# Kernel optimization log

Measured on AMD Instinct MI355X. Metric: run time of the kernel, lower is better.

The kernel has to match this reference:

```python
import jax, jax.numpy as jnp
import numpy as np
from jax import lax

NGTH = 15  # num_gth_mem
EPS = 1e-5  # BatchNorm eps


def _conv(x, w, b):
    y = lax.conv_general_dilated(x, w, (1, 1), 'VALID',
                                 dimension_numbers=('NCHW', 'OIHW', 'NCHW'))
    return y + b[None, :, None, None]


def _bn(x, g, b, m, v):
    # eval-mode BatchNorm2d with running stats
    return g[None, :, None, None] * (x - m[None, :, None, None]) * lax.rsqrt(v[None, :, None, None] + EPS) + b[None, :, None, None]


def _masked_stats(x, w):
    # x: (B, M, ...) ; w: (B, M) float weights. Population mean/std over masked mem slots.
    extra = (1,) * (x.ndim - 2)
    we = w.reshape(w.shape[:2] + extra)
    cnt = jnp.sum(w, axis=1).reshape((w.shape[0],) + extra)
    s = jnp.sum(x * we, axis=1)
    ss = jnp.sum(x * x * we, axis=1)
    mean = s / cnt
    var = jnp.maximum(ss / cnt - mean * mean, 0.0)
    return mean, jnp.sqrt(var)


def _forward(target_scores, ptm, pmt, predicted_iou, mem_mask, params):
    nf, ns, nmem, c, h, w = ptm.shape
    B = nf * ns
    ts = target_scores.reshape(B, 1, h, w)
    pmt = pmt.reshape(B, nmem, 1, h, w)
    ptm = ptm.reshape(B, nmem, c, h, w)
    mask = mem_mask.reshape(B, nmem)
    piou = predicted_iou.reshape(B, 1, 1, 1)

    mf = mask.astype(ts.dtype)
    # rank of each selected slot within the masked (ordered) selection
    rank = jnp.cumsum(mf, axis=1) - 1.0
    gth_w = mf * (rank < NGTH).astype(ts.dtype)   # first NGTH selected slots
    oth_w = mf * (rank >= NGTH).astype(ts.dtype)  # remaining selected slots

    max_ts = jnp.max(ts.reshape(B, -1), axis=1)

    pmt_mean, pmt_std = _masked_stats(pmt, mf)                 # (B,1,h,w)
    pmt_gth = pmt[:, :NGTH]                                    # unmasked slice (as in torch code)
    pmt_gth_mean = jnp.mean(pmt_gth, axis=1)
    pmt_gth_std = jnp.std(pmt_gth, axis=1)
    pmt_oth_mean, pmt_oth_std = _masked_stats(pmt, oth_w)

    ptm_max = jnp.max(ptm.reshape(B, nmem, -1), axis=2)        # (B, nmem)
    m_mm, s_mm = _masked_stats(ptm_max, mf)
    m_gm, s_gm = _masked_stats(ptm_max, gth_w)
    m_om, s_om = _masked_stats(ptm_max, oth_w)

    def bcast(v):
        return jnp.broadcast_to(v.reshape(B, 1, 1, 1), (B, 1, h, w))

    inp = jnp.concatenate([
        bcast(max_ts), jnp.broadcast_to(piou, (B, 1, h, w)),
        pmt_mean, pmt_std, pmt_gth_mean, pmt_gth_std, pmt_oth_mean, pmt_oth_std,
        bcast(m_mm), bcast(s_mm), bcast(m_gm), bcast(s_gm), bcast(m_om), bcast(s_om)
    ], axis=1)  # (B, 14, h, w)

    (c1w, c1b, g1, b1, m1, v1, c2w, c2b, g2, b2, m2, v2,
     c3w, c3b, g3, b3, m3, v3, c4w, c4b) = params
    x = jax.nn.relu(_bn(_conv(inp, c1w, c1b), g1, b1, m1, v1))
    x = lax.reduce_window(x, -jnp.inf, lax.max, (1, 1, 2, 2), (1, 1, 2, 2), 'VALID')
    x = jax.nn.relu(_bn(_conv(x, c2w, c2b), g2, b2, m2, v2))
    x = jax.nn.relu(_bn(_conv(x, c3w, c3b), g3, b3, m3, v3))
    x = _conv(x, c4w, c4b)
    return jnp.max(x, axis=(2, 3), keepdims=True)  # AdaptiveMaxPool2d((1,1)) -> (B,1,1,1)


def setup_inputs() -> dict:
    key = jax.random.key(0)
    ks = jax.random.split(key, 16)
    nf, ns, nmem, h, w = 16, 32, 30, 32, 32
    d = {}
    d['target_scores'] = jax.random.normal(ks[0], (nf, ns, 1, h, w), jnp.float32)
    d['ptm'] = jax.random.uniform(ks[1], (nf, ns, nmem, 1, h, w), jnp.float32)
    d['pmt'] = jax.random.uniform(ks[2], (nf, ns, nmem, 1, h, w), jnp.float32)
    d['predicted_iou'] = jax.random.uniform(ks[3], (nf, ns), jnp.float32)
    mask = jax.random.uniform(ks[4], (nf, ns, nmem)) < 0.7
    mask = mask.at[..., :20].set(True)  # >= 20 selected -> 'other' set non-empty
    d['mem_mask'] = mask
    d['conv1_w'] = jax.random.normal(ks[5], (64, 14, 3, 3), jnp.float32) * 0.1
    d['conv1_b'] = jnp.zeros((64,), jnp.float32)
    d['bn1_g'] = jnp.ones((64,), jnp.float32); d['bn1_b'] = jnp.zeros((64,), jnp.float32)
    d['bn1_m'] = jnp.zeros((64,), jnp.float32); d['bn1_v'] = jnp.ones((64,), jnp.float32)
    d['conv2_w'] = jax.random.normal(ks[6], (64, 64, 3, 3), jnp.float32) * 0.05
    d['conv2_b'] = jnp.zeros((64,), jnp.float32)
    d['bn2_g'] = jnp.ones((64,), jnp.float32); d['bn2_b'] = jnp.zeros((64,), jnp.float32)
    d['bn2_m'] = jnp.zeros((64,), jnp.float32); d['bn2_v'] = jnp.ones((64,), jnp.float32)
    d['conv3_w'] = jax.random.normal(ks[7], (64, 64, 3, 3), jnp.float32) * 0.05
    d['conv3_b'] = jnp.zeros((64,), jnp.float32)
    d['bn3_g'] = jnp.ones((64,), jnp.float32); d['bn3_b'] = jnp.zeros((64,), jnp.float32)
    d['bn3_m'] = jnp.zeros((64,), jnp.float32); d['bn3_v'] = jnp.ones((64,), jnp.float32)
    d['conv4_w'] = jax.random.normal(ks[8], (1, 64, 3, 3), jnp.float32) * 0.05
    d['conv4_b'] = jnp.zeros((1,), jnp.float32)
    return d


def reference(target_scores, ptm, pmt, predicted_iou, mem_mask,
              conv1_w, conv1_b, bn1_g, bn1_b, bn1_m, bn1_v,
              conv2_w, conv2_b, bn2_g, bn2_b, bn2_m, bn2_v,
              conv3_w, conv3_b, bn3_g, bn3_b, bn3_m, bn3_v,
              conv4_w, conv4_b):
    params = (conv1_w, conv1_b, bn1_g, bn1_b, bn1_m, bn1_v,
              conv2_w, conv2_b, bn2_g, bn2_b, bn2_m, bn2_v,
              conv3_w, conv3_b, bn3_g, bn3_b, bn3_m, bn3_v,
              conv4_w, conv4_b)
    return _forward(target_scores, ptm, pmt, predicted_iou, mem_mask, params)
```

## Files before the change

kernel.cpp:

```cpp
#include <hip/hip_runtime.h>
#include <math.h>

#define NFB  512
#define NMEM 30
#define PIX  1024
#define EPSF 1e-5f

typedef _Float16 half8_t __attribute__((ext_vector_type(8)));
typedef _Float16 half4_t __attribute__((ext_vector_type(4)));
typedef float float4_t __attribute__((ext_vector_type(4)));

#define OFF_SCAL  8388608
#define OFF_PMAX  8413184
#define OFF_WPAIR 8474624
#define OFF_X1H   8597504
#define OFF_X2H   24326144
#define OFF_X3H   37957632
#define OFF_W2R   49491968
#define OFF_W3R   49565696
#define OFF_WR1   49639424
#define OFF_WSUM1 49651712

__global__ __launch_bounds__(256) void k_repack(
    const float* __restrict__ w, _Float16* __restrict__ wr)
{
  int i = blockIdx.x * 256 + threadIdx.x;
  if (i < 36864) {
    int kr = i / 12288;
    int rem = i - kr * 12288;
    int oc = rem / 192;
    int k = rem - oc * 192;
    int kc = k >> 6, ci = k & 63;
    wr[i] = (_Float16)w[((oc * 64 + ci) * 3 + kr) * 3 + kc];
  }
}

__global__ __launch_bounds__(256) void k_repack1(
    const float* __restrict__ w, _Float16* __restrict__ wr1,
    float* __restrict__ wsum1)
{
  int i = blockIdx.x * 256 + threadIdx.x;
  if (i < 6144) {
    int kr = i / 2048;
    int rem = i - kr * 2048;
    int oc = rem >> 5;
    int k = rem & 31;
    int kc = k >> 3, ci = k & 7;
    _Float16 v = (_Float16)0.f;
    if (kc < 3 && ci < 6)
      v = (_Float16)w[((oc * 14 + (2 + ci)) * 3 + kr) * 3 + kc];
    wr1[i] = v;
  } else if (i < 6144 + 512) {
    int j = i - 6144;
    int oc = j >> 3, u = j & 7;
    const int uch[8] = {0, 1, 8, 9, 10, 11, 12, 13};
    const float* wp = w + (oc * 14 + uch[u]) * 9;
    float s = 0.f;
    #pragma unroll
    for (int k = 0; k < 9; ++k) s += wp[k];
    wsum1[j] = s;
  }
}

__global__ __launch_bounds__(256) void kA_ptm_max(
    const float* __restrict__ ptm, float* __restrict__ pmax)
{
  const int t = threadIdx.x, lane = t & 63, wave = t >> 6;
  const int w = blockIdx.x * 4 + wave;
  const float* p = ptm + (size_t)w * PIX;
  float4 v0 = *(const float4*)(p + lane * 4);
  float4 v1 = *(const float4*)(p + lane * 4 + 256);
  float4 v2 = *(const float4*)(p + lane * 4 + 512);
  float4 v3 = *(const float4*)(p + lane * 4 + 768);
  float mx = fmaxf(fmaxf(fmaxf(v0.x, v0.y), fmaxf(v0.z, v0.w)),
                   fmaxf(fmaxf(v1.x, v1.y), fmaxf(v1.z, v1.w)));
  mx = fmaxf(mx, fmaxf(fmaxf(fmaxf(v2.x, v2.y), fmaxf(v2.z, v2.w)),
                       fmaxf(fmaxf(v3.x, v3.y), fmaxf(v3.z, v3.w))));
  #pragma unroll
  for (int off = 32; off > 0; off >>= 1)
    mx = fmaxf(mx, __shfl_down(mx, off, 64));
  if (lane == 0) pmax[w] = mx;
}

__global__ __launch_bounds__(256) void kB_scal(
    const float* __restrict__ ts, const float* __restrict__ piou,
    const int* __restrict__ mask, const float* __restrict__ pmax,
    float* __restrict__ scal12, float2* __restrict__ wpair)
{
  const int b = blockIdx.x, t = threadIdx.x, lane = t & 63, wave = t >> 6;
  __shared__ float s_red[4];
  {
    float4 v = ((const float4*)(ts + (size_t)b * PIX))[t];
    float mx = fmaxf(fmaxf(v.x, v.y), fmaxf(v.z, v.w));
    #pragma unroll
    for (int off = 32; off > 0; off >>= 1)
      mx = fmaxf(mx, __shfl_down(mx, off, 64));
    if (lane == 0) s_red[wave] = mx;
  }
  __syncthreads();
  if (t == 0) {
    float maxts = fmaxf(fmaxf(s_red[0], s_red[1]), fmaxf(s_red[2], s_red[3]));
    float wm[NMEM], wo[NMEM];
    float cum = 0.f, cm = 0.f, cg = 0.f, co = 0.f;
    #pragma unroll
    for (int m = 0; m < NMEM; ++m) {
      float f  = (mask[b * NMEM + m] != 0) ? 1.f : 0.f;
      float gg = (cum < 15.f) ? f : 0.f;
      float oo = f - gg;
      cum += f;
      wm[m] = f; wo[m] = oo;
      cm += f; cg += gg; co += oo;
    }
    const float* px = pmax + b * NMEM;
    float sm = 0, sm2 = 0, sg = 0, sg2 = 0, so = 0, so2 = 0;
    #pragma unroll
    for (int m = 0; m < NMEM; ++m) {
      float x = px[m];
      float gg = wm[m] - wo[m];
      sm += wm[m] * x;  sm2 += wm[m] * x * x;
      sg += gg * x;     sg2 += gg * x * x;
      so += wo[m] * x;  so2 += wo[m] * x * x;
      wpair[b * NMEM + m] = make_float2(wm[m], wo[m]);
    }
    float a = sm / cm, g = sg / cg, o = so / co;
    float* sp = scal12 + b * 12;
    sp[0] = maxts; sp[1] = piou[b];
    sp[2] = a; sp[3] = sqrtf(fmaxf(sm2 / cm - a * a, 0.f));
    sp[4] = g; sp[5] = sqrtf(fmaxf(sg2 / cg - g * g, 0.f));
    sp[6] = o; sp[7] = sqrtf(fmaxf(so2 / co - o * o, 0.f));
    sp[8] = cm; sp[9] = cg; sp[10] = co; sp[11] = 0.f;
  }
}

__global__ __launch_bounds__(256) void kC_pmt_stats(
    const float* __restrict__ pmt, const float2* __restrict__ wpair,
    const float* __restrict__ scal12, _Float16* __restrict__ img6h)
{
  const int b = blockIdx.x, t = threadIdx.x;
  __shared__ float s_wm[NMEM], s_wo[NMEM];
  if (t < NMEM) {
    float2 wv = wpair[b * NMEM + t];
    s_wm[t] = wv.x; s_wo[t] = wv.y;
  }
  __syncthreads();
  const float cm = scal12[b * 12 + 8];
  const float co = scal12[b * 12 + 10];
  const int p0 = t * 4;
  const float* pb = pmt + (size_t)b * NMEM * PIX + p0;

  float sA[4] = {0,0,0,0}, qA[4] = {0,0,0,0};
  float sG[4] = {0,0,0,0}, qG[4] = {0,0,0,0};
  float sO[4] = {0,0,0,0}, qO[4] = {0,0,0,0};

  #pragma unroll 1
  for (int mb = 0; mb < 15; mb += 5) {
    float4 v[5];
    #pragma unroll
    for (int j = 0; j < 5; ++j) v[j] = *(const float4*)(pb + (size_t)(mb + j) * PIX);
    #pragma unroll
    for (int j = 0; j < 5; ++j) {
      float wm = s_wm[mb + j], wo = s_wo[mb + j];
      float xv[4] = {v[j].x, v[j].y, v[j].z, v[j].w};
      #pragma unroll
      for (int k = 0; k < 4; ++k) {
        float x = xv[k];
        sA[k] = fmaf(wm, x, sA[k]); qA[k] = fmaf(wm * x, x, qA[k]);
        sO[k] = fmaf(wo, x, sO[k]); qO[k] = fmaf(wo * x, x, qO[k]);
        sG[k] += x; qG[k] = fmaf(x, x, qG[k]);
      }
    }
  }
  #pragma unroll 1
  for (int mb = 15; mb < 30; mb += 5) {
    float4 v[5];
    #pragma unroll
    for (int j = 0; j < 5; ++j) v[j] = *(const float4*)(pb + (size_t)(mb + j) * PIX);
    #pragma unroll
    for (int j = 0; j < 5; ++j) {
      float wm = s_wm[mb + j], wo = s_wo[mb + j];
      float xv[4] = {v[j].x, v[j].y, v[j].z, v[j].w};
      #pragma unroll
      for (int k = 0; k < 4; ++k) {
        float x = xv[k];
        sA[k] = fmaf(wm, x, sA[k]); qA[k] = fmaf(wm * x, x, qA[k]);
        sO[k] = fmaf(wo, x, sO[k]); qO[k] = fmaf(wo * x, x, qO[k]);
      }
    }
  }

  half8_t* ob = (half8_t*)(img6h + (size_t)b * 8192 + (size_t)p0 * 8);
  #pragma unroll
  for (int j = 0; j < 4; ++j) {
    float m0 = sA[j] / cm;   float d0 = sqrtf(fmaxf(qA[j] / cm - m0 * m0, 0.f));
    float m1 = sG[j] / 15.f; float d1 = sqrtf(fmaxf(qG[j] / 15.f - m1 * m1, 0.f));
    float m2 = sO[j] / co;   float d2 = sqrtf(fmaxf(qO[j] / co - m2 * m2, 0.f));
    half8_t v;
    v[0] = (_Float16)m0; v[1] = (_Float16)d0;
    v[2] = (_Float16)m1; v[3] = (_Float16)d1;
    v[4] = (_Float16)m2; v[5] = (_Float16)d2;
    v[6] = (_Float16)0.f; v[7] = (_Float16)0.f;
    ob[j] = v;
  }
}

__global__ __launch_bounds__(256) void k1_conv1_mfma(
    const _Float16* __restrict__ img6h, const float* __restrict__ scal12,
    const _Float16* __restrict__ wr1, const float* __restrict__ wsum1,
    const float* __restrict__ bias, const float* __restrict__ gam,
    const float* __restrict__ bet, const float* __restrict__ mu,
    const float* __restrict__ var, _Float16* __restrict__ x1h)
{
  __shared__ _Float16 s_img[1028 * 8];
  const int b = blockIdx.x, t = threadIdx.x, lane = t & 63, wave = t >> 6;
  const int n16 = lane & 15, q = lane >> 4;
  {
    const half8_t* src = (const half8_t*)(img6h + (size_t)b * 8192);
    half8_t* dst = (half8_t*)s_img;
    for (int i = t; i < 1024; i += 256) dst[i] = src[i];
    if (t < 4) {
      half8_t z = {(_Float16)0.f, (_Float16)0.f, (_Float16)0.f, (_Float16)0.f,
                   (_Float16)0.f, (_Float16)0.f, (_Float16)0.f, (_Float16)0.f};
      dst[1024 + t] = z;
    }
  }

  const int ocA = wave * 16 + n16;
  half8_t af[3];
  #pragma unroll
  for (int kr = 0; kr < 3; ++kr)
    af[kr] = *(const half8_t*)(wr1 + (kr * 64 + ocA) * 32 + q * 8);

  const int oc0 = wave * 16 + q * 4;
  float scv[4], shv[4], cst[4];
  {
    const float* sp = scal12 + b * 12;
    #pragma unroll
    for (int rg = 0; rg < 4; ++rg) {
      int oc = oc0 + rg;
      float s = gam[oc] * rsqrtf(var[oc] + EPSF);
      scv[rg] = s;
      shv[rg] = (bias[oc] - mu[oc]) * s + bet[oc];
      float c = 0.f;
      #pragma unroll
      for (int u = 0; u < 8; ++u) c = fmaf(wsum1[oc * 8 + u], sp[u], c);
      cst[rg] = c;
    }
  }
  __syncthreads();

  #pragma unroll 1
  for (int pr = 0; pr < 15; ++pr) {
    const int r0 = pr * 2;
    float4_t acc[2][2];
    #pragma unroll
    for (int row = 0; row < 2; ++row)
      #pragma unroll
      for (int tt = 0; tt < 2; ++tt)
        acc[row][tt] = (float4_t){0.f, 0.f, 0.f, 0.f};
    #pragma unroll
    for (int row = 0; row < 2; ++row) {
      #pragma unroll
      for (int kr = 0; kr < 3; ++kr) {
        const int ip = (r0 + row + kr) * 32 + n16 + q;
        #pragma unroll
        for (int tt = 0; tt < 2; ++tt) {
          half8_t bf = *(const half8_t*)(s_img + (ip + tt * 16) * 8);
          acc[row][tt] = __builtin_amdgcn_mfma_f32_16x16x32_f16(
              af[kr], bf, acc[row][tt], 0, 0, 0);
        }
      }
    }
    #pragma unroll
    for (int tt = 0; tt < 2; ++tt) {
      float mm[4];
      #pragma unroll
      for (int j = 0; j < 4; ++j) {
        float m = fmaxf(acc[0][tt][j], acc[1][tt][j]);
        mm[j] = fmaxf(m, __shfl_xor(m, 1, 64));
      }
      if ((n16 & 1) == 0) {
        int pc = tt * 8 + (n16 >> 1);
        half4_t v;
        if (pc < 15) {
          #pragma unroll
          for (int rg = 0; rg < 4; ++rg)
            v[rg] = (_Float16)fmaxf(scv[rg] * (mm[rg] + cst[rg]) + shv[rg], 0.f);
        } else {
          v[0] = (_Float16)0.f; v[1] = (_Float16)0.f;
          v[2] = (_Float16)0.f; v[3] = (_Float16)0.f;
        }
        *(half4_t*)(x1h + ((((size_t)b * 15 + pr) * 16) + pc) * 64 + oc0) = v;
      }
    }
  }
}

template<int IH, int OW, int NT>
__global__ __launch_bounds__(256, 3) void k_conv_mfma(
    const _Float16* __restrict__ xin, const _Float16* __restrict__ wrep,
    const float* __restrict__ bias, const float* __restrict__ gam,
    const float* __restrict__ bet, const float* __restrict__ mu,
    const float* __restrict__ var, _Float16* __restrict__ xout)
{
  constexpr int NPIX = OW * OW;
  constexpr int NIN = IH * 16;
  __shared__ _Float16 s_in[NIN * 72 + 8];
  const int b = blockIdx.x, t = threadIdx.x;
  const int lane = t & 63, wave = t >> 6;
  const int n16 = lane & 15, q = lane >> 4;

  {
    const half8_t* src = (const half8_t*)(xin + (size_t)b * NIN * 64);
    half8_t* dst = (half8_t*)s_in;
    for (int g = t; g < NIN * 8; g += 256) {
      int pix = g >> 3, cib = g & 7;
      dst[pix * 9 + cib] = src[g];
    }
  }

  int base72[NT];
  #pragma unroll
  for (int nt = 0; nt < NT; ++nt) {
    int p = nt * 16 + n16;
    int pe = (p < NPIX) ? p : (NPIX - 1);
    int r = pe / OW, c = pe - r * OW;
    base72[nt] = (r * 16 + c) * 72;
  }

  float4_t acc[NT];
  #pragma unroll
  for (int nt = 0; nt < NT; ++nt) acc[nt] = (float4_t){0.f, 0.f, 0.f, 0.f};

  const int ocA = wave * 16 + n16;
  __syncthreads();

  #pragma unroll 1
  for (int kr = 0; kr < 3; ++kr) {
    half8_t af[6];
    const half8_t* wp = (const half8_t*)(wrep + (size_t)(kr * 64 + ocA) * 192 + q * 8);
    #pragma unroll
    for (int ks = 0; ks < 6; ++ks) af[ks] = wp[ks * 4];
    const int krbase = kr * (16 * 72);
    #pragma unroll
    for (int ks = 0; ks < 6; ++ks) {
      const int k0 = ks * 32 + q * 8;
      const int kadd = krbase + (k0 >> 6) * 72 + (k0 & 63);
      #pragma unroll
      for (int nt = 0; nt < NT; ++nt) {
        half8_t bf = *(const half8_t*)(s_in + base72[nt] + kadd);
        acc[nt] = __builtin_amdgcn_mfma_f32_16x16x32_f16(af[ks], bf, acc[nt], 0, 0, 0);
      }
    }
  }

  const int ocb = wave * 16 + q * 4;
  float scv[4], shv[4];
  #pragma unroll
  for (int rg = 0; rg < 4; ++rg) {
    int o = ocb + rg;
    float s = gam[o] * rsqrtf(var[o] + EPSF);
    scv[rg] = s;
    shv[rg] = (bias[o] - mu[o]) * s + bet[o];
  }
  #pragma unroll
  for (int nt = 0; nt < NT; ++nt) {
    int p = nt * 16 + n16;
    if (p < NPIX) {
      int r = p / OW, c = p - r * OW;
      half4_t v;
      #pragma unroll
      for (int rg = 0; rg < 4; ++rg)
        v[rg] = (_Float16)fmaxf(acc[nt][rg] * scv[rg] + shv[rg], 0.f);
      *(half4_t*)(xout + (((size_t)b * OW + r) * 16 + c) * 64 + ocb) = v;
    }
  }
}

__global__ __launch_bounds__(128) void k4_conv4max(
    const _Float16* __restrict__ x3, const float* __restrict__ w4,
    const float* __restrict__ b4, float* __restrict__ out)
{
  __shared__ _Float16 s_in[11 * 16 * 72 + 8];
  __shared__ float s_w[9][64];
  __shared__ float s_red[2];
  const int b = blockIdx.x, t = threadIdx.x;
  {
    const half8_t* src = (const half8_t*)(x3 + (size_t)b * 11 * 16 * 64);
    half8_t* dst = (half8_t*)s_in;
    for (int g = t; g < 11 * 16 * 8; g += 128) {
      int pix = g >> 3, cib = g & 7;
      dst[pix * 9 + cib] = src[g];
    }
  }
  for (int i = t; i < 576; i += 128) {
    int ci = i / 9, k = i - ci * 9;
    s_w[k][ci] = w4[i];
  }
  __syncthreads();
  float val = -INFINITY;
  if (t < 81) {
    const int r = t / 9, c = t - (t / 9) * 9;
    float acc = 0.f;
    #pragma unroll
    for (int kr = 0; kr < 3; ++kr)
      #pragma unroll
      for (int kc = 0; kc < 3; ++kc) {
        const _Float16* ip = s_in + ((r + kr) * 16 + (c + kc)) * 72;
        const float* wk = s_w[kr * 3 + kc];
        #pragma unroll
        for (int cig = 0; cig < 8; ++cig) {
          half8_t x = *(const half8_t*)(ip + cig * 8);
          #pragma unroll
          for (int j = 0; j < 8; ++j)
            acc = fmaf((float)x[j], wk[cig * 8 + j], acc);
        }
      }
    val = acc;
  }
  #pragma unroll
  for (int off = 32; off > 0; off >>= 1)
    val = fmaxf(val, __shfl_down(val, off, 64));
  if ((t & 63) == 0) s_red[t >> 6] = val;
  __syncthreads();
  if (t == 0) out[b] = fmaxf(s_red[0], s_red[1]) + b4[0];
}

extern "C" void kernel_launch(void* const* d_in, const int* in_sizes, int n_in,
                              void* d_out, int out_size, void* d_ws, size_t ws_size,
                              hipStream_t stream) {
  const float* ts   = (const float*)d_in[0];
  const float* ptm  = (const float*)d_in[1];
  const float* pmt  = (const float*)d_in[2];
  const float* piou = (const float*)d_in[3];
  const int*   mask = (const int*)d_in[4];
  const float* c1w = (const float*)d_in[5];
  const float* c1b = (const float*)d_in[6];
  const float* g1  = (const float*)d_in[7];
  const float* b1  = (const float*)d_in[8];
  const float* m1  = (const float*)d_in[9];
  const float* v1  = (const float*)d_in[10];
  const float* c2w = (const float*)d_in[11];
  const float* c2b = (const float*)d_in[12];
  const float* g2  = (const float*)d_in[13];
  const float* b2  = (const float*)d_in[14];
  const float* m2  = (const float*)d_in[15];
  const float* v2  = (const float*)d_in[16];
  const float* c3w = (const float*)d_in[17];
  const float* c3b = (const float*)d_in[18];
  const float* g3  = (const float*)d_in[19];
  const float* b3  = (const float*)d_in[20];
  const float* m3  = (const float*)d_in[21];
  const float* v3  = (const float*)d_in[22];
  const float* c4w = (const float*)d_in[23];
  const float* c4b = (const float*)d_in[24];

  char* ws = (char*)d_ws;
  _Float16*  img6h  = (_Float16*)ws;
  float*     scal12 = (float*)(ws + OFF_SCAL);
  float*     pmax   = (float*)(ws + OFF_PMAX);
  float2*    wpair  = (float2*)(ws + OFF_WPAIR);
  _Float16*  x1h    = (_Float16*)(ws + OFF_X1H);
  _Float16*  x2h    = (_Float16*)(ws + OFF_X2H);
  _Float16*  x3h    = (_Float16*)(ws + OFF_X3H);
  _Float16*  w2rep  = (_Float16*)(ws + OFF_W2R);
  _Float16*  w3rep  = (_Float16*)(ws + OFF_W3R);
  _Float16*  wr1    = (_Float16*)(ws + OFF_WR1);
  float*     wsum1  = (float*)(ws + OFF_WSUM1);

  k_repack<<<144, 256, 0, stream>>>(c2w, w2rep);
  k_repack<<<144, 256, 0, stream>>>(c3w, w3rep);
  k_repack1<<<26, 256, 0, stream>>>(c1w, wr1, wsum1);
  kA_ptm_max<<<NFB * NMEM / 4, 256, 0, stream>>>(ptm, pmax);
  kB_scal<<<NFB, 256, 0, stream>>>(ts, piou, mask, pmax, scal12, wpair);
  kC_pmt_stats<<<NFB, 256, 0, stream>>>(pmt, wpair, scal12, img6h);
  k1_conv1_mfma<<<NFB, 256, 0, stream>>>(img6h, scal12, wr1, wsum1,
                                         c1b, g1, b1, m1, v1, x1h);
  k_conv_mfma<15, 13, 11><<<NFB, 256, 0, stream>>>(x1h, w2rep, c2b, g2, b2, m2, v2, x2h);
  k_conv_mfma<13, 11, 8><<<NFB, 256, 0, stream>>>(x2h, w3rep, c3b, g3, b3, m3, v3, x3h);
  k4_conv4max<<<NFB, 128, 0, stream>>>(x3h, c4w, c4b, (float*)d_out);
}
```

Measured before the change: 262.8 us.

## Fuse stats, conv1-3 and conv4-max into one per-batch megakernel

Merges the three weight-repack kernels into a single prep launch, and fuses ptm max, scalar stats, pmt stats, conv1, conv2, conv3 and conv4+max into one kernel with one block per batch item. Intermediates stay in shared memory, except conv2 output, which round-trips through a workspace buffer. This removes most global intermediate traffic and about eight launches. In exchange it uses a large shared buffer (~58KB) that limits occupancy, and the stats and convolution phases now run serially inside each block rather than overlapping across blocks.

```diff
diff --git a/kernel.cpp b/kernel.cpp
--- a/kernel.cpp
+++ b/kernel.cpp
@@ -10,51 +10,43 @@
 typedef _Float16 half4_t __attribute__((ext_vector_type(4)));
 typedef float float4_t __attribute__((ext_vector_type(4)));
 
-#define OFF_SCAL  8388608
-#define OFF_PMAX  8413184
-#define OFF_WPAIR 8474624
-#define OFF_X1H   8597504
-#define OFF_X2H   24326144
-#define OFF_X3H   37957632
-#define OFF_W2R   49491968
-#define OFF_W3R   49565696
-#define OFF_WR1   49639424
-#define OFF_WSUM1 49651712
-
-__global__ __launch_bounds__(256) void k_repack(
-    const float* __restrict__ w, _Float16* __restrict__ wr)
+#define OFF_W2R   13631488
+#define OFF_W3R   13705216
+#define OFF_WR1   13778944
+#define OFF_WSUM1 13791232
+
+__global__ __launch_bounds__(256) void k_prep(
+    const float* __restrict__ c1w, const float* __restrict__ c2w,
+    const float* __restrict__ c3w, _Float16* __restrict__ w2rep,
+    _Float16* __restrict__ w3rep, _Float16* __restrict__ wr1,
+    float* __restrict__ wsum1)
 {
   int i = blockIdx.x * 256 + threadIdx.x;
   if (i < 36864) {
-    int kr = i / 12288;
-    int rem = i - kr * 12288;
-    int oc = rem / 192;
-    int k = rem - oc * 192;
+    int kr = i / 12288, rem = i - kr * 12288;
+    int oc = rem / 192, k = rem - oc * 192;
     int kc = k >> 6, ci = k & 63;
-    wr[i] = (_Float16)w[((oc * 64 + ci) * 3 + kr) * 3 + kc];
-  }
-}
-
-__global__ __launch_bounds__(256) void k_repack1(
-    const float* __restrict__ w, _Float16* __restrict__ wr1,
-    float* __restrict__ wsum1)
-{
-  int i = blockIdx.x * 256 + threadIdx.x;
-  if (i < 6144) {
-    int kr = i / 2048;
-    int rem = i - kr * 2048;
-    int oc = rem >> 5;
-    int k = rem & 31;
+    w2rep[i] = (_Float16)c2w[((oc * 64 + ci) * 3 + kr) * 3 + kc];
+  } else if (i < 73728) {
+    int j = i - 36864;
+    int kr = j / 12288, rem = j - kr * 12288;
+    int oc = rem / 192, k = rem - oc * 192;
+    int kc = k >> 6, ci = k & 63;
+    w3rep[j] = (_Float16)c3w[((oc * 64 + ci) * 3 + kr) * 3 + kc];
+  } else if (i < 79872) {
+    int j = i - 73728;
+    int kr = j / 2048, rem = j - kr * 2048;
+    int oc = rem >> 5, k = rem & 31;
     int kc = k >> 3, ci = k & 7;
     _Float16 v = (_Float16)0.f;
     if (kc < 3 && ci < 6)
-      v = (_Float16)w[((oc * 14 + (2 + ci)) * 3 + kr) * 3 + kc];
-    wr1[i] = v;
-  } else if (i < 6144 + 512) {
-    int j = i - 6144;
+      v = (_Float16)c1w[((oc * 14 + (2 + ci)) * 3 + kr) * 3 + kc];
+    wr1[j] = v;
+  } else if (i < 80384) {
+    int j = i - 79872;
     int oc = j >> 3, u = j & 7;
     const int uch[8] = {0, 1, 8, 9, 10, 11, 12, 13};
-    const float* wp = w + (oc * 14 + uch[u]) * 9;
+    const float* wp = c1w + (oc * 14 + uch[u]) * 9;
     float s = 0.f;
     #pragma unroll
     for (int k = 0; k < 9; ++k) s += wp[k];
@@ -62,367 +54,374 @@
   }
 }
 
-__global__ __launch_bounds__(256) void kA_ptm_max(
-    const float* __restrict__ ptm, float* __restrict__ pmax)
+__global__ __launch_bounds__(256, 2) void k_mega(
+    const float* __restrict__ ts, const float* __restrict__ ptm,
+    const float* __restrict__ pmt, const float* __restrict__ piou,
+    const int* __restrict__ mask,
+    const _Float16* __restrict__ wr1, const float* __restrict__ wsum1,
+    const float* __restrict__ c1b, const float* __restrict__ g1,
+    const float* __restrict__ b1, const float* __restrict__ m1,
+    const float* __restrict__ v1,
+    const _Float16* __restrict__ w2rep,
+    const float* __restrict__ c2b, const float* __restrict__ g2,
+    const float* __restrict__ b2, const float* __restrict__ m2,
+    const float* __restrict__ v2,
+    const _Float16* __restrict__ w3rep,
+    const float* __restrict__ c3b, const float* __restrict__ g3,
+    const float* __restrict__ b3, const float* __restrict__ m3,
+    const float* __restrict__ v3,
+    const float* __restrict__ c4w, const float* __restrict__ c4b,
+    _Float16* __restrict__ x2h, float* __restrict__ out)
 {
-  const int t = threadIdx.x, lane = t & 63, wave = t >> 6;
-  const int w = blockIdx.x * 4 + wave;
-  const float* p = ptm + (size_t)w * PIX;
-  float4 v0 = *(const float4*)(p + lane * 4);
-  float4 v1 = *(const float4*)(p + lane * 4 + 256);
-  float4 v2 = *(const float4*)(p + lane * 4 + 512);
-  float4 v3 = *(const float4*)(p + lane * 4 + 768);
-  float mx = fmaxf(fmaxf(fmaxf(v0.x, v0.y), fmaxf(v0.z, v0.w)),
-                   fmaxf(fmaxf(v1.x, v1.y), fmaxf(v1.z, v1.w)));
-  mx = fmaxf(mx, fmaxf(fmaxf(fmaxf(v2.x, v2.y), fmaxf(v2.z, v2.w)),
-                       fmaxf(fmaxf(v3.x, v3.y), fmaxf(v3.z, v3.w))));
-  #pragma unroll
-  for (int off = 32; off > 0; off >>= 1)
-    mx = fmaxf(mx, __shfl_down(mx, off, 64));
-  if (lane == 0) pmax[w] = mx;
-}
-
-__global__ __launch_bounds__(256) void kB_scal(
-    const float* __restrict__ ts, const float* __restrict__ piou,
-    const int* __restrict__ mask, const float* __restrict__ pmax,
-    float* __restrict__ scal12, float2* __restrict__ wpair)
-{
-  const int b = blockIdx.x, t = threadIdx.x, lane = t & 63, wave = t >> 6;
-  __shared__ float s_red[4];
-  {
-    float4 v = ((const float4*)(ts + (size_t)b * PIX))[t];
-    float mx = fmaxf(fmaxf(v.x, v.y), fmaxf(v.z, v.w));
-    #pragma unroll
-    for (int off = 32; off > 0; off >>= 1)
-      mx = fmaxf(mx, __shfl_down(mx, off, 64));
-    if (lane == 0) s_red[wave] = mx;
-  }
-  __syncthreads();
+  __shared__ __align__(16) char s_buf[55296];
+  __shared__ float s_wm[NMEM], s_wo[NMEM], s_pmax[NMEM];
+  __shared__ float s_red[4], s_scal[12], s_cnt[4];
+  __shared__ float s_w4[576];
+
+  const int b = blockIdx.x, t = threadIdx.x;
+  const int lane = t & 63, wave = t >> 6;
+  const int n16 = lane & 15, q = lane >> 4;
+  _Float16* const IMG = (_Float16*)s_buf;
+  _Float16* const X1  = (_Float16*)(s_buf + 16448);
+  _Float16* const X2S = (_Float16*)s_buf;
+  _Float16* const X3  = (_Float16*)(s_buf + 29952);
+
+  for (int i = t; i < 576; i += 256) {
+    int ci = i / 9, k = i - ci * 9;
+    s_w4[k * 64 + ci] = c4w[i];
+  }
   if (t == 0) {
-    float maxts = fmaxf(fmaxf(s_red[0], s_red[1]), fmaxf(s_red[2], s_red[3]));
-    float wm[NMEM], wo[NMEM];
     float cum = 0.f, cm = 0.f, cg = 0.f, co = 0.f;
-    #pragma unroll
     for (int m = 0; m < NMEM; ++m) {
       float f  = (mask[b * NMEM + m] != 0) ? 1.f : 0.f;
       float gg = (cum < 15.f) ? f : 0.f;
       float oo = f - gg;
       cum += f;
-      wm[m] = f; wo[m] = oo;
+      s_wm[m] = f; s_wo[m] = oo;
       cm += f; cg += gg; co += oo;
     }
-    const float* px = pmax + b * NMEM;
+    s_cnt[0] = cm; s_cnt[1] = cg; s_cnt[2] = co;
+  }
+  for (int m = wave; m < NMEM; m += 4) {
+    const float* p = ptm + ((size_t)b * NMEM + m) * PIX;
+    float4 v0 = *(const float4*)(p + lane * 4);
+    float4 v1_ = *(const float4*)(p + lane * 4 + 256);
+    float4 v2_ = *(const float4*)(p + lane * 4 + 512);
+    float4 v3_ = *(const float4*)(p + lane * 4 + 768);
+    float mx = fmaxf(fmaxf(fmaxf(v0.x, v0.y), fmaxf(v0.z, v0.w)),
+                     fmaxf(fmaxf(v1_.x, v1_.y), fmaxf(v1_.z, v1_.w)));
+    mx = fmaxf(mx, fmaxf(fmaxf(fmaxf(v2_.x, v2_.y), fmaxf(v2_.z, v2_.w)),
+                         fmaxf(fmaxf(v3_.x, v3_.y), fmaxf(v3_.z, v3_.w))));
+    #pragma unroll
+    for (int off = 32; off > 0; off >>= 1)
+      mx = fmaxf(mx, __shfl_down(mx, off, 64));
+    if (lane == 0) s_pmax[m] = mx;
+  }
+  {
+    float4 v = ((const float4*)(ts + (size_t)b * PIX))[t];
+    float mx = fmaxf(fmaxf(v.x, v.y), fmaxf(v.z, v.w));
+    #pragma unroll
+    for (int off = 32; off > 0; off >>= 1)
+      mx = fmaxf(mx, __shfl_down(mx, off, 64));
+    if (lane == 0) s_red[wave] = mx;
+  }
+  __syncthreads();
+  if (t == 0) {
+    float maxts = fmaxf(fmaxf(s_red[0], s_red[1]), fmaxf(s_red[2], s_red[3]));
     float sm = 0, sm2 = 0, sg = 0, sg2 = 0, so = 0, so2 = 0;
-    #pragma unroll
     for (int m = 0; m < NMEM; ++m) {
-      float x = px[m];
-      float gg = wm[m] - wo[m];
-      sm += wm[m] * x;  sm2 += wm[m] * x * x;
-      sg += gg * x;     sg2 += gg * x * x;
-      so += wo[m] * x;  so2 += wo[m] * x * x;
-      wpair[b * NMEM + m] = make_float2(wm[m], wo[m]);
-    }
+      float x = s_pmax[m];
+      float gg = s_wm[m] - s_wo[m];
+      sm += s_wm[m] * x;  sm2 += s_wm[m] * x * x;
+      sg += gg * x;       sg2 += gg * x * x;
+      so += s_wo[m] * x;  so2 += s_wo[m] * x * x;
+    }
+    float cm = s_cnt[0], cg = s_cnt[1], co = s_cnt[2];
     float a = sm / cm, g = sg / cg, o = so / co;
-    float* sp = scal12 + b * 12;
-    sp[0] = maxts; sp[1] = piou[b];
-    sp[2] = a; sp[3] = sqrtf(fmaxf(sm2 / cm - a * a, 0.f));
-    sp[4] = g; sp[5] = sqrtf(fmaxf(sg2 / cg - g * g, 0.f));
-    sp[6] = o; sp[7] = sqrtf(fmaxf(so2 / co - o * o, 0.f));
-    sp[8] = cm; sp[9] = cg; sp[10] = co; sp[11] = 0.f;
-  }
-}
-
-__global__ __launch_bounds__(256) void kC_pmt_stats(
-    const float* __restrict__ pmt, const float2* __restrict__ wpair,
-    const float* __restrict__ scal12, _Float16* __restrict__ img6h)
-{
-  const int b = blockIdx.x, t = threadIdx.x;
-  __shared__ float s_wm[NMEM], s_wo[NMEM];
-  if (t < NMEM) {
-    float2 wv = wpair[b * NMEM + t];
-    s_wm[t] = wv.x; s_wo[t] = wv.y;
-  }
-  __syncthreads();
-  const float cm = scal12[b * 12 + 8];
-  const float co = scal12[b * 12 + 10];
-  const int p0 = t * 4;
-  const float* pb = pmt + (size_t)b * NMEM * PIX + p0;
-
-  float sA[4] = {0,0,0,0}, qA[4] = {0,0,0,0};
-  float sG[4] = {0,0,0,0}, qG[4] = {0,0,0,0};
-  float sO[4] = {0,0,0,0}, qO[4] = {0,0,0,0};
-
-  #pragma unroll 1
-  for (int mb = 0; mb < 15; mb += 5) {
-    float4 v[5];
-    #pragma unroll
-    for (int j = 0; j < 5; ++j) v[j] = *(const float4*)(pb + (size_t)(mb + j) * PIX);
-    #pragma unroll
-    for (int j = 0; j < 5; ++j) {
-      float wm = s_wm[mb + j], wo = s_wo[mb + j];
-      float xv[4] = {v[j].x, v[j].y, v[j].z, v[j].w};
-      #pragma unroll
-      for (int k = 0; k < 4; ++k) {
-        float x = xv[k];
-        sA[k] = fmaf(wm, x, sA[k]); qA[k] = fmaf(wm * x, x, qA[k]);
-        sO[k] = fmaf(wo, x, sO[k]); qO[k] = fmaf(wo * x, x, qO[k]);
-        sG[k] += x; qG[k] = fmaf(x, x, qG[k]);
-      }
-    }
-  }
-  #pragma unroll 1
-  for (int mb = 15; mb < 30; mb += 5) {
-    float4 v[5];
-    #pragma unroll
-    for (int j = 0; j < 5; ++j) v[j] = *(const float4*)(pb + (size_t)(mb + j) * PIX);
-    #pragma unroll
-    for (int j = 0; j < 5; ++j) {
-      float wm = s_wm[mb + j], wo = s_wo[mb + j];
-      float xv[4] = {v[j].x, v[j].y, v[j].z, v[j].w};
-      #pragma unroll
-      for (int k = 0; k < 4; ++k) {
-        float x = xv[k];
-        sA[k] = fmaf(wm, x, sA[k]); qA[k] = fmaf(wm * x, x, qA[k]);
-        sO[k] = fmaf(wo, x, sO[k]); qO[k] = fmaf(wo * x, x, qO[k]);
-      }
-    }
-  }
-
-  half8_t* ob = (half8_t*)(img6h + (size_t)b * 8192 + (size_t)p0 * 8);
-  #pragma unroll
-  for (int j = 0; j < 4; ++j) {
-    float m0 = sA[j] / cm;   float d0 = sqrtf(fmaxf(qA[j] / cm - m0 * m0, 0.f));
-    float m1 = sG[j] / 15.f; float d1 = sqrtf(fmaxf(qG[j] / 15.f - m1 * m1, 0.f));
-    float m2 = sO[j] / co;   float d2 = sqrtf(fmaxf(qO[j] / co - m2 * m2, 0.f));
-    half8_t v;
-    v[0] = (_Float16)m0; v[1] = (_Float16)d0;
-    v[2] = (_Float16)m1; v[3] = (_Float16)d1;
-    v[4] = (_Float16)m2; v[5] = (_Float16)d2;
-    v[6] = (_Float16)0.f; v[7] = (_Float16)0.f;
-    ob[j] = v;
-  }
-}
-
-__global__ __launch_bounds__(256) void k1_conv1_mfma(
-    const _Float16* __restrict__ img6h, const float* __restrict__ scal12,
-    const _Float16* __restrict__ wr1, const float* __restrict__ wsum1,
-    const float* __restrict__ bias, const float* __restrict__ gam,
-    const float* __restrict__ bet, const float* __restrict__ mu,
-    const float* __restrict__ var, _Float16* __restrict__ x1h)
-{
-  __shared__ _Float16 s_img[1028 * 8];
-  const int b = blockIdx.x, t = threadIdx.x, lane = t & 63, wave = t >> 6;
-  const int n16 = lane & 15, q = lane >> 4;
-  {
-    const half8_t* src = (const half8_t*)(img6h + (size_t)b * 8192);
-    half8_t* dst = (half8_t*)s_img;
-    for (int i = t; i < 1024; i += 256) dst[i] = src[i];
+    s_scal[0] = maxts; s_scal[1] = piou[b];
+    s_scal[2] = a; s_scal[3] = sqrtf(fmaxf(sm2 / cm - a * a, 0.f));
+    s_scal[4] = g; s_scal[5] = sqrtf(fmaxf(sg2 / cg - g * g, 0.f));
+    s_scal[6] = o; s_scal[7] = sqrtf(fmaxf(so2 / co - o * o, 0.f));
+  }
+  {
+    const float cm = s_cnt[0], co = s_cnt[2];
+    const int p0 = t * 4;
+    const float* pb = pmt + (size_t)b * NMEM * PIX + p0;
+    float sA[4] = {0,0,0,0}, qA[4] = {0,0,0,0};
+    float sG[4] = {0,0,0,0}, qG[4] = {0,0,0,0};
+    float sO[4] = {0,0,0,0}, qO[4] = {0,0,0,0};
+    #pragma unroll 1
+    for (int mb = 0; mb < 15; mb += 5) {
+      float4 v[5];
+      #pragma unroll
+      for (int j = 0; j < 5; ++j) v[j] = *(const float4*)(pb + (size_t)(mb + j) * PIX);
+      #pragma unroll
+      for (int j = 0; j < 5; ++j) {
+        float wm = s_wm[mb + j], wo = s_wo[mb + j];
+        float xv[4] = {v[j].x, v[j].y, v[j].z, v[j].w};
+        #pragma unroll
+        for (int k = 0; k < 4; ++k) {
+          float x = xv[k];
+          sA[k] = fmaf(wm, x, sA[k]); qA[k] = fmaf(wm * x, x, qA[k]);
+          sO[k] = fmaf(wo, x, sO[k]); qO[k] = fmaf(wo * x, x, qO[k]);
+          sG[k] += x; qG[k] = fmaf(x, x, qG[k]);
+        }
+      }
+    }
+    #pragma unroll 1
+    for (int mb = 15; mb < 30; mb += 5) {
+      float4 v[5];
+      #pragma unroll
+      for (int j = 0; j < 5; ++j) v[j] = *(const float4*)(pb + (size_t)(mb + j) * PIX);
+      #pragma unroll
+      for (int j = 0; j < 5; ++j) {
+        float wm = s_wm[mb + j], wo = s_wo[mb + j];
+        float xv[4] = {v[j].x, v[j].y, v[j].z, v[j].w};
+        #pragma unroll
+        for (int k = 0; k < 4; ++k) {
+          float x = xv[k];
+          sA[k] = fmaf(wm, x, sA[k]); qA[k] = fmaf(wm * x, x, qA[k]);
+          sO[k] = fmaf(wo, x, sO[k]); qO[k] = fmaf(wo * x, x, qO[k]);
+        }
+      }
+    }
+    half8_t* ob = (half8_t*)(IMG) + p0;
+    #pragma unroll
+    for (int j = 0; j < 4; ++j) {
+      float m0 = sA[j] / cm;   float d0 = sqrtf(fmaxf(qA[j] / cm - m0 * m0, 0.f));
+      float m1_ = sG[j] / 15.f; float d1 = sqrtf(fmaxf(qG[j] / 15.f - m1_ * m1_, 0.f));
+      float m2_ = sO[j] / co;   float d2 = sqrtf(fmaxf(qO[j] / co - m2_ * m2_, 0.f));
+      half8_t v;
+      v[0] = (_Float16)m0;  v[1] = (_Float16)d0;
+      v[2] = (_Float16)m1_; v[3] = (_Float16)d1;
+      v[4] = (_Float16)m2_; v[5] = (_Float16)d2;
+      v[6] = (_Float16)0.f; v[7] = (_Float16)0.f;
+      ob[j] = v;
+    }
     if (t < 4) {
-      half8_t z = {(_Float16)0.f, (_Float16)0.f, (_Float16)0.f, (_Float16)0.f,
-                   (_Float16)0.f, (_Float16)0.f, (_Float16)0.f, (_Float16)0.f};
-      dst[1024 + t] = z;
-    }
-  }
-
-  const int ocA = wave * 16 + n16;
-  half8_t af[3];
-  #pragma unroll
-  for (int kr = 0; kr < 3; ++kr)
-    af[kr] = *(const half8_t*)(wr1 + (kr * 64 + ocA) * 32 + q * 8);
-
-  const int oc0 = wave * 16 + q * 4;
-  float scv[4], shv[4], cst[4];
-  {
-    const float* sp = scal12 + b * 12;
+      half8_t z = {(_Float16)0.f,(_Float16)0.f,(_Float16)0.f,(_Float16)0.f,
+                   (_Float16)0.f,(_Float16)0.f,(_Float16)0.f,(_Float16)0.f};
+      ((half8_t*)IMG)[1024 + t] = z;
+    }
+  }
+  __syncthreads();
+
+  {
+    const int ocA = wave * 16 + n16;
+    half8_t af[3];
+    #pragma unroll
+    for (int kr = 0; kr < 3; ++kr)
+      af[kr] = *(const half8_t*)(wr1 + (kr * 64 + ocA) * 32 + q * 8);
+    const int oc0 = wave * 16 + q * 4;
+    float scv[4], shv[4], cst[4];
     #pragma unroll
     for (int rg = 0; rg < 4; ++rg) {
       int oc = oc0 + rg;
-      float s = gam[oc] * rsqrtf(var[oc] + EPSF);
+      float s = g1[oc] * rsqrtf(v1[oc] + EPSF);
       scv[rg] = s;
-      shv[rg] = (bias[oc] - mu[oc]) * s + bet[oc];
+      shv[rg] = (c1b[oc] - m1[oc]) * s + b1[oc];
       float c = 0.f;
       #pragma unroll
-      for (int u = 0; u < 8; ++u) c = fmaf(wsum1[oc * 8 + u], sp[u], c);
+      for (int u = 0; u < 8; ++u) c = fmaf(wsum1[oc * 8 + u], s_scal[u], c);
       cst[rg] = c;
     }
-  }
-  __syncthreads();
-
-  #pragma unroll 1
-  for (int pr = 0; pr < 15; ++pr) {
-    const int r0 = pr * 2;
-    float4_t acc[2][2];
-    #pragma unroll
-    for (int row = 0; row < 2; ++row)
-      #pragma unroll
-      for (int tt = 0; tt < 2; ++tt)
-        acc[row][tt] = (float4_t){0.f, 0.f, 0.f, 0.f};
-    #pragma unroll
-    for (int row = 0; row < 2; ++row) {
-      #pragma unroll
-      for (int kr = 0; kr < 3; ++kr) {
-        const int ip = (r0 + row + kr) * 32 + n16 + q;
-        #pragma unroll
-        for (int tt = 0; tt < 2; ++tt) {
-          half8_t bf = *(const half8_t*)(s_img + (ip + tt * 16) * 8);
-          acc[row][tt] = __builtin_amdgcn_mfma_f32_16x16x32_f16(
-              af[kr], bf, acc[row][tt], 0, 0, 0);
-        }
-      }
-    }
-    #pragma unroll
-    for (int tt = 0; tt < 2; ++tt) {
-      float mm[4];
-      #pragma unroll
-      for (int j = 0; j < 4; ++j) {
-        float m = fmaxf(acc[0][tt][j], acc[1][tt][j]);
-        mm[j] = fmaxf(m, __shfl_xor(m, 1, 64));
-      }
-      if ((n16 & 1) == 0) {
-        int pc = tt * 8 + (n16 >> 1);
-        half4_t v;
-        if (pc < 15) {
+    #pragma unroll 1
+    for (int pr = 0; pr < 15; ++pr) {
+      const int r0 = pr * 2;
+      float4_t acc[2][2];
+      #pragma unroll
+      for (int row = 0; row < 2; ++row)
+        #pragma unroll
+        for (int tt = 0; tt < 2; ++tt)
+          acc[row][tt] = (float4_t){0.f, 0.f, 0.f, 0.f};
+      #pragma unroll
+      for (int row = 0; row < 2; ++row) {
+        #pragma unroll
+        for (int kr = 0; kr < 3; ++kr) {
+          const int ip = (r0 + row + kr) * 32 + n16 + q;
           #pragma unroll
-          for (int rg = 0; rg < 4; ++rg)
-            v[rg] = (_Float16)fmaxf(scv[rg] * (mm[rg] + cst[rg]) + shv[rg], 0.f);
-        } else {
-          v[0] = (_Float16)0.f; v[1] = (_Float16)0.f;
-          v[2] = (_Float16)0.f; v[3] = (_Float16)0.f;
-        }
-        *(half4_t*)(x1h + ((((size_t)b * 15 + pr) * 16) + pc) * 64 + oc0) = v;
-      }
-    }
-  }
-}
-
-template<int IH, int OW, int NT>
-__global__ __launch_bounds__(256, 3) void k_conv_mfma(
-    const _Float16* __restrict__ xin, const _Float16* __restrict__ wrep,
-    const float* __restrict__ bias, const float* __restrict__ gam,
-    const float* __restrict__ bet, const float* __restrict__ mu,
-    const float* __restrict__ var, _Float16* __restrict__ xout)
-{
-  constexpr int NPIX = OW * OW;
-  constexpr int NIN = IH * 16;
-  __shared__ _Float16 s_in[NIN * 72 + 8];
-  const int b = blockIdx.x, t = threadIdx.x;
-  const int lane = t & 63, wave = t >> 6;
-  const int n16 = lane & 15, q = lane >> 4;
-
-  {
-    const half8_t* src = (const half8_t*)(xin + (size_t)b * NIN * 64);
-    half8_t* dst = (half8_t*)s_in;
-    for (int g = t; g < NIN * 8; g += 256) {
+          for (int tt = 0; tt < 2; ++tt) {
+            half8_t bf = *(const half8_t*)(IMG + (ip + tt * 16) * 8);
+            acc[row][tt] = __builtin_amdgcn_mfma_f32_16x16x32_f16(
+                af[kr], bf, acc[row][tt], 0, 0, 0);
+          }
+        }
+      }
+      #pragma unroll
+      for (int tt = 0; tt < 2; ++tt) {
+        float mm[4];
+        #pragma unroll
+        for (int j = 0; j < 4; ++j) {
+          float m = fmaxf(acc[0][tt][j], acc[1][tt][j]);
+          mm[j] = fmaxf(m, __shfl_xor(m, 1, 64));
+        }
+        if ((n16 & 1) == 0) {
+          int pc = tt * 8 + (n16 >> 1);
+          half4_t vv;
+          if (pc < 15) {
+            #pragma unroll
+            for (int rg = 0; rg < 4; ++rg)
+              vv[rg] = (_Float16)fmaxf(scv[rg] * (mm[rg] + cst[rg]) + shv[rg], 0.f);
+          } else {
+            vv[0] = (_Float16)0.f; vv[1] = (_Float16)0.f;
+            vv[2] = (_Float16)0.f; vv[3] = (_Float16)0.f;
+          }
+          *(half4_t*)(X1 + (pr * 16 + pc) * 72 + oc0) = vv;
+        }
+      }
+    }
+  }
+  __syncthreads();
+
+  {
+    int base72[11];
+    #pragma unroll
+    for (int nt = 0; nt < 11; ++nt) {
+      int p = nt * 16 + n16;
+      int pe = (p < 169) ? p : 168;
+      int r = pe / 13, c = pe - r * 13;
+      base72[nt] = (r * 16 + c) * 72;
+    }
+    float4_t acc[11];
+    #pragma unroll
+    for (int nt = 0; nt < 11; ++nt) acc[nt] = (float4_t){0.f, 0.f, 0.f, 0.f};
+    const int ocA = wave * 16 + n16;
+    #pragma unroll 1
+    for (int kr = 0; kr < 3; ++kr) {
+      half8_t af[6];
+      const half8_t* wp = (const half8_t*)(w2rep + (size_t)(kr * 64 + ocA) * 192 + q * 8);
+      #pragma unroll
+      for (int ks = 0; ks < 6; ++ks) af[ks] = wp[ks * 4];
+      const int krbase = kr * (16 * 72);
+      #pragma unroll
+      for (int ks = 0; ks < 6; ++ks) {
+        const int k0 = ks * 32 + q * 8;
+        const int kadd = krbase + (k0 >> 6) * 72 + (k0 & 63);
+        #pragma unroll
+        for (int nt = 0; nt < 11; ++nt) {
+          half8_t bf = *(const half8_t*)(X1 + base72[nt] + kadd);
+          acc[nt] = __builtin_amdgcn_mfma_f32_16x16x32_f16(af[ks], bf, acc[nt], 0, 0, 0);
+        }
+      }
+    }
+    const int ocb = wave * 16 + q * 4;
+    float scv[4], shv[4];
+    #pragma unroll
+    for (int rg = 0; rg < 4; ++rg) {
+      int o = ocb + rg;
+      float s = g2[o] * rsqrtf(v2[o] + EPSF);
+      scv[rg] = s;
+      shv[rg] = (c2b[o] - m2[o]) * s + b2[o];
+    }
+    #pragma unroll
+    for (int nt = 0; nt < 11; ++nt) {
+      int p = nt * 16 + n16;
+      if (p < 169) {
+        int r = p / 13, c = p - r * 13;
+        half4_t vv;
+        #pragma unroll
+        for (int rg = 0; rg < 4; ++rg)
+          vv[rg] = (_Float16)fmaxf(acc[nt][rg] * scv[rg] + shv[rg], 0.f);
+        *(half4_t*)(x2h + (((size_t)b * 13 + r) * 16 + c) * 64 + ocb) = vv;
+      }
+    }
+  }
+  __threadfence_block();
+  __syncthreads();
+  {
+    const half8_t* src = (const half8_t*)(x2h + (size_t)b * 13 * 16 * 64);
+    half8_t* dst = (half8_t*)X2S;
+    for (int g = t; g < 208 * 8; g += 256) {
       int pix = g >> 3, cib = g & 7;
       dst[pix * 9 + cib] = src[g];
     }
   }
-
-  int base72[NT];
-  #pragma unroll
-  for (int nt = 0; nt < NT; ++nt) {
-    int p = nt * 16 + n16;
-    int pe = (p < NPIX) ? p : (NPIX - 1);
-    int r = pe / OW, c = pe - r * OW;
-    base72[nt] = (r * 16 + c) * 72;
-  }
-
-  float4_t acc[NT];
-  #pragma unroll
-  for (int nt = 0; nt < NT; ++nt) acc[nt] = (float4_t){0.f, 0.f, 0.f, 0.f};
-
-  const int ocA = wave * 16 + n16;
-  __syncthreads();
-
-  #pragma unroll 1
-  for (int kr = 0; kr < 3; ++kr) {
-    half8_t af[6];
-    const half8_t* wp = (const half8_t*)(wrep + (size_t)(kr * 64 + ocA) * 192 + q * 8);
-    #pragma unroll
-    for (int ks = 0; ks < 6; ++ks) af[ks] = wp[ks * 4];
-    const int krbase = kr * (16 * 72);
-    #pragma unroll
-    for (int ks = 0; ks < 6; ++ks) {
-      const int k0 = ks * 32 + q * 8;
-      const int kadd = krbase + (k0 >> 6) * 72 + (k0 & 63);
-      #pragma unroll
-      for (int nt = 0; nt < NT; ++nt) {
-        half8_t bf = *(const half8_t*)(s_in + base72[nt] + kadd);
-        acc[nt] = __builtin_amdgcn_mfma_f32_16x16x32_f16(af[ks], bf, acc[nt], 0, 0, 0);
-      }
-    }
-  }
-
-  const int ocb = wave * 16 + q * 4;
-  float scv[4], shv[4];
-  #pragma unroll
-  for (int rg = 0; rg < 4; ++rg) {
-    int o = ocb + rg;
-    float s = gam[o] * rsqrtf(var[o] + EPSF);
-    scv[rg] = s;
-    shv[rg] = (bias[o] - mu[o]) * s + bet[o];
-  }
-  #pragma unroll
-  for (int nt = 0; nt < NT; ++nt) {
-    int p = nt * 16 + n16;
-    if (p < NPIX) {
-      int r = p / OW, c = p - r * OW;
-      half4_t v;
-      #pragma unroll
-      for (int rg = 0; rg < 4; ++rg)
-        v[rg] = (_Float16)fmaxf(acc[nt][rg] * scv[rg] + shv[rg], 0.f);
-      *(half4_t*)(xout + (((size_t)b * OW + r) * 16 + c) * 64 + ocb) = v;
-    }
-  }
-}
-
-__global__ __launch_bounds__(128) void k4_conv4max(
-    const _Float16* __restrict__ x3, const float* __restrict__ w4,
-    const float* __restrict__ b4, float* __restrict__ out)
-{
-  __shared__ _Float16 s_in[11 * 16 * 72 + 8];
-  __shared__ float s_w[9][64];
-  __shared__ float s_red[2];
-  const int b = blockIdx.x, t = threadIdx.x;
-  {
-    const half8_t* src = (const half8_t*)(x3 + (size_t)b * 11 * 16 * 64);
-    half8_t* dst = (half8_t*)s_in;
-    for (int g = t; g < 11 * 16 * 8; g += 128) {
-      int pix = g >> 3, cib = g & 7;
-      dst[pix * 9 + cib] = src[g];
-    }
-  }
-  for (int i = t; i < 576; i += 128) {
-    int ci = i / 9, k = i - ci * 9;
-    s_w[k][ci] = w4[i];
-  }
-  __syncthreads();
-  float val = -INFINITY;
-  if (t < 81) {
-    const int r = t / 9, c = t - (t / 9) * 9;
-    float acc = 0.f;
-    #pragma unroll
-    for (int kr = 0; kr < 3; ++kr)
-      #pragma unroll
-      for (int kc = 0; kc < 3; ++kc) {
-        const _Float16* ip = s_in + ((r + kr) * 16 + (c + kc)) * 72;
-        const float* wk = s_w[kr * 3 + kc];
-        #pragma unroll
-        for (int cig = 0; cig < 8; ++cig) {
-          half8_t x = *(const half8_t*)(ip + cig * 8);
+  __syncthreads();
+
+  {
+    int base72[8];
+    #pragma unroll
+    for (int nt = 0; nt < 8; ++nt) {
+      int p = nt * 16 + n16;
+      int pe = (p < 121) ? p : 120;
+      int r = pe / 11, c = pe - r * 11;
+      base72[nt] = (r * 16 + c) * 72;
+    }
+    float4_t acc[8];
+    #pragma unroll
+    for (int nt = 0; nt < 8; ++nt) acc[nt] = (float4_t){0.f, 0.f, 0.f, 0.f};
+    const int ocA = wave * 16 + n16;
+    #pragma unroll 1
+    for (int kr = 0; kr < 3; ++kr) {
+      half8_t af[6];
+      const half8_t* wp = (const half8_t*)(w3rep + (size_t)(kr * 64 + ocA) * 192 + q * 8);
+      #pragma unroll
+      for (int ks = 0; ks < 6; ++ks) af[ks] = wp[ks * 4];
+      const int krbase = kr * (16 * 72);
+      #pragma unroll
+      for (int ks = 0; ks < 6; ++ks) {
+        const int k0 = ks * 32 + q * 8;
+        const int kadd = krbase + (k0 >> 6) * 72 + (k0 & 63);
+        #pragma unroll
+        for (int nt = 0; nt < 8; ++nt) {
+          half8_t bf = *(const half8_t*)(X2S + base72[nt] + kadd);
+          acc[nt] = __builtin_amdgcn_mfma_f32_16x16x32_f16(af[ks], bf, acc[nt], 0, 0, 0);
+        }
+      }
+    }
+    const int ocb = wave * 16 + q * 4;
+    float scv[4], shv[4];
+    #pragma unroll
+    for (int rg = 0; rg < 4; ++rg) {
+      int o = ocb + rg;
+      float s = g3[o] * rsqrtf(v3[o] + EPSF);
+      scv[rg] = s;
+      shv[rg] = (c3b[o] - m3[o]) * s + b3[o];
+    }
+    #pragma unroll
+    for (int nt = 0; nt < 8; ++nt) {
+      int p = nt * 16 + n16;
+      if (p < 121) {
+        int r = p / 11, c = p - r * 11;
+        half4_t vv;
+        #pragma unroll
+        for (int rg = 0; rg < 4; ++rg)
+          vv[rg] = (_Float16)fmaxf(acc[nt][rg] * scv[rg] + shv[rg], 0.f);
+        *(half4_t*)(X3 + (r * 16 + c) * 72 + ocb) = vv;
+      }
+    }
+  }
+  __syncthreads();
+
+  {
+    float val = -INFINITY;
+    if (t < 81) {
+      const int r = t / 9, c = t - (t / 9) * 9;
+      float acc = 0.f;
+      #pragma unroll
+      for (int kr = 0; kr < 3; ++kr)
+        #pragma unroll
+        for (int kc = 0; kc < 3; ++kc) {
+          const _Float16* ip = X3 + ((r + kr) * 16 + (c + kc)) * 72;
+          const float* wk = s_w4 + (kr * 3 + kc) * 64;
           #pragma unroll
-          for (int j = 0; j < 8; ++j)
-            acc = fmaf((float)x[j], wk[cig * 8 + j], acc);
-        }
-      }
-    val = acc;
-  }
-  #pragma unroll
-  for (int off = 32; off > 0; off >>= 1)
-    val = fmaxf(val, __shfl_down(val, off, 64));
-  if ((t & 63) == 0) s_red[t >> 6] = val;
-  __syncthreads();
-  if (t == 0) out[b] = fmaxf(s_red[0], s_red[1]) + b4[0];
+          for (int cig = 0; cig < 8; ++cig) {
+            half8_t x = *(const half8_t*)(ip + cig * 8);
+            #pragma unroll
+            for (int j = 0; j < 8; ++j)
+              acc = fmaf((float)x[j], wk[cig * 8 + j], acc);
+          }
+        }
+      val = acc;
+    }
+    #pragma unroll
+    for (int off = 32; off > 0; off >>= 1)
+      val = fmaxf(val, __shfl_down(val, off, 64));
+    if (lane == 0) s_red[wave] = val;
+    __syncthreads();
+    if (t == 0)
+      out[b] = fmaxf(fmaxf(s_red[0], s_red[1]), fmaxf(s_red[2], s_red[3])) + c4b[0];
+  }
 }
 
 extern "C" void kernel_launch(void* const* d_in, const int* in_sizes, int n_in,
@@ -455,27 +454,17 @@
   const float* c4b = (const float*)d_in[24];
 
   char* ws = (char*)d_ws;
-  _Float16*  img6h  = (_Float16*)ws;
-  float*     scal12 = (float*)(ws + OFF_SCAL);
-  float*     pmax   = (float*)(ws + OFF_PMAX);
-  float2*    wpair  = (float2*)(ws + OFF_WPAIR);
-  _Float16*  x1h    = (_Float16*)(ws + OFF_X1H);
-  _Float16*  x2h    = (_Float16*)(ws + OFF_X2H);
-  _Float16*  x3h    = (_Float16*)(ws + OFF_X3H);
-  _Float16*  w2rep  = (_Float16*)(ws + OFF_W2R);
-  _Float16*  w3rep  = (_Float16*)(ws + OFF_W3R);
-  _Float16*  wr1    = (_Float16*)(ws + OFF_WR1);
-  float*     wsum1  = (float*)(ws + OFF_WSUM1);
-
-  k_repack<<<144, 256, 0, stream>>>(c2w, w2rep);
-  k_repack<<<144, 256, 0, stream>>>(c3w, w3rep);
-  k_repack1<<<26, 256, 0, stream>>>(c1w, wr1, wsum1);
-  kA_ptm_max<<<NFB * NMEM / 4, 256, 0, stream>>>(ptm, pmax);
-  kB_scal<<<NFB, 256, 0, stream>>>(ts, piou, mask, pmax, scal12, wpair);
-  kC_pmt_stats<<<NFB, 256, 0, stream>>>(pmt, wpair, scal12, img6h);
-  k1_conv1_mfma<<<NFB, 256, 0, stream>>>(img6h, scal12, wr1, wsum1,
-                                         c1b, g1, b1, m1, v1, x1h);
-  k_conv_mfma<15, 13, 11><<<NFB, 256, 0, stream>>>(x1h, w2rep, c2b, g2, b2, m2, v2, x2h);
-  k_conv_mfma<13, 11, 8><<<NFB, 256, 0, stream>>>(x2h, w3rep, c3b, g3, b3, m3, v3, x3h);
-  k4_conv4max<<<NFB, 128, 0, stream>>>(x3h, c4w, c4b, (float*)d_out);
+  _Float16*  x2h   = (_Float16*)ws;
+  _Float16*  w2rep = (_Float16*)(ws + OFF_W2R);
+  _Float16*  w3rep = (_Float16*)(ws + OFF_W3R);
+  _Float16*  wr1   = (_Float16*)(ws + OFF_WR1);
+  float*     wsum1 = (float*)(ws + OFF_WSUM1);
+
+  k_prep<<<314, 256, 0, stream>>>(c1w, c2w, c3w, w2rep, w3rep, wr1, wsum1);
+  k_mega<<<NFB, 256, 0, stream>>>(
+      ts, ptm, pmt, piou, mask,
+      wr1, wsum1, c1b, g1, b1, m1, v1,
+      w2rep, c2b, g2, b2, m2, v2,
+      w3rep, c3b, g3, b3, m3, v3,
+      c4w, c4b, x2h, (float*)d_out);
 }
```

After: 225.4 us. -14.2%, faster.
